# Performance work log

Hardware: AMD Instinct MI355X
Metric: run time of the kernel (lower is better)

Reference implementation:

```python
import jax, jax.numpy as jnp
import numpy as np

HEADS = 4
NEG_SLOPE = 0.2  # GATv2Conv default negative_slope and module's LeakyReLU
LN_EPS = 1e-5


def setup_inputs() -> dict:
    key = jax.random.key(0)
    ks = jax.random.split(key, 12)
    N, D, E = 50000, 128, 400000
    H, C = HEADS, D
    s = 0.05
    x = jax.random.normal(ks[0], (N, D), dtype=jnp.float32)
    edge_index = jax.random.randint(ks[1], (2, E), 0, N, dtype=jnp.int64)
    return {
        "x": x,
        "edge_index": edge_index,
        "W_l": jax.random.normal(ks[2], (D, H * C), dtype=jnp.float32) * s,
        "b_l": jnp.zeros((H * C,), jnp.float32),
        "W_r": jax.random.normal(ks[3], (D, H * C), dtype=jnp.float32) * s,
        "b_r": jnp.zeros((H * C,), jnp.float32),
        "att": jax.random.normal(ks[4], (H, C), dtype=jnp.float32) * s,
        "gat_bias": jnp.zeros((C,), jnp.float32),
        "ln_g": jnp.ones((D,), jnp.float32),
        "ln_b": jnp.zeros((D,), jnp.float32),
        "W1": jax.random.normal(ks[5], (D, 2 * D), dtype=jnp.float32) * s,
        "b1": jnp.zeros((2 * D,), jnp.float32),
        "W2": jax.random.normal(ks[6], (2 * D, D), dtype=jnp.float32) * s,
        "b2": jnp.zeros((D,), jnp.float32),
    }


def _gatv2(x, src, dst, W_l, b_l, W_r, b_r, att, gat_bias, N):
    D = x.shape[1]
    H, C = HEADS, D
    xl = (x @ W_l + b_l).reshape(N, H, C)  # source-side projection
    xr = (x @ W_r + b_r).reshape(N, H, C)  # target-side projection
    # per-edge GATv2 score: leaky_relu(x_j + x_i) . att
    e = jax.nn.leaky_relu(xl[src] + xr[dst], NEG_SLOPE)  # [E, H, C]
    alpha = jnp.einsum('ehc,hc->eh', e, att)             # [E, H]
    # segment softmax over destination nodes
    amax = jax.ops.segment_max(alpha, dst, num_segments=N)  # [N, H]
    ex = jnp.exp(alpha - amax[dst])
    denom = jax.ops.segment_sum(ex, dst, num_segments=N)
    w = ex / (denom[dst] + 1e-16)                        # [E, H]
    msg = xl[src] * w[:, :, None]                        # [E, H, C]
    out = jax.ops.segment_sum(msg, dst, num_segments=N)  # [N, H, C]
    return out.mean(axis=1) + gat_bias                   # concat=False -> head mean + bias


def reference(x, edge_index, W_l, b_l, W_r, b_r, att, gat_bias, ln_g, ln_b, W1, b1, W2, b2):
    N = x.shape[0]
    # GATv2Conv default add_self_loops=True
    loops = jnp.arange(N, dtype=edge_index.dtype)
    src = jnp.concatenate([edge_index[0], loops])
    dst = jnp.concatenate([edge_index[1], loops])
    h = x + _gatv2(x, src, dst, W_l, b_l, W_r, b_r, att, gat_bias, N)
    # LayerNorm
    mu = h.mean(-1, keepdims=True)
    var = ((h - mu) ** 2).mean(-1, keepdims=True)
    hn = (h - mu) * jax.lax.rsqrt(var + LN_EPS) * ln_g + ln_b
    # FFN with residual
    ffn = jax.nn.leaky_relu(hn @ W1 + b1, NEG_SLOPE) @ W2 + b2
    return hn + ffn
```

## Files before the change

kernel.cpp:

```cpp
#include <hip/hip_runtime.h>
#include <hip/hip_bf16.h>
#include <stdint.h>

typedef __hip_bfloat16 bf16;
typedef __attribute__((ext_vector_type(8))) short short8;
typedef __attribute__((ext_vector_type(4))) float f32x4;

#define NEG 0.2f
#define LN_EPS 1e-5f

__device__ __host__ __forceinline__ int stdch(int q) {
    return (q & ~63) | (16 * (q & 3)) | ((q & 63) >> 2);
}

__device__ __forceinline__ float bits2f(unsigned b) {
    return __uint_as_float(b << 16);
}
__device__ __forceinline__ float hi2f(unsigned b) {
    return __uint_as_float(b & 0xffff0000u);
}
__device__ __forceinline__ unsigned short f2b_bits(float f) {
    unsigned u = __float_as_uint(f);
    unsigned r = u + 0x7fffu + ((u >> 16) & 1u);
    return (unsigned short)(r >> 16);
}
__device__ __forceinline__ float lrelu(float v) {
    return fmaxf(v, 0.f) + NEG * fminf(v, 0.f);
}
__device__ __forceinline__ void unpack8(uint4 u, float* v) {
    v[0] = bits2f(u.x); v[1] = hi2f(u.x);
    v[2] = bits2f(u.y); v[3] = hi2f(u.y);
    v[4] = bits2f(u.z); v[5] = hi2f(u.z);
    v[6] = bits2f(u.w); v[7] = hi2f(u.w);
}

union S8 { uint4 u; short8 s; unsigned short us[8]; };
__device__ __forceinline__ short8 ld8b(const char* p) {
    S8 c; c.u = *(const uint4*)p; return c.s;
}
__device__ __forceinline__ short8 ld8f(const float* p) {
    float4 a = ((const float4*)p)[0], b = ((const float4*)p)[1];
    S8 c;
    c.us[0] = f2b_bits(a.x); c.us[1] = f2b_bits(a.y);
    c.us[2] = f2b_bits(a.z); c.us[3] = f2b_bits(a.w);
    c.us[4] = f2b_bits(b.x); c.us[5] = f2b_bits(b.y);
    c.us[6] = f2b_bits(b.z); c.us[7] = f2b_bits(b.w);
    return c.s;
}

__global__ void detect_kernel(const unsigned* __restrict__ xw, const int* __restrict__ ei,
                              int* __restrict__ flags, int E) {
    int lane = threadIdx.x;
    int sane = 0;
    for (int k = 0; k < 4; ++k) {
        unsigned short lo = (unsigned short)(xw[k * 64 + lane] & 0xFFFFu);
        int ex = (lo >> 7) & 0xFF;
        if (lo == 0 || (ex > 100 && ex < 155)) sane++;
    }
#pragma unroll
    for (int off = 32; off > 0; off >>= 1) sane += __shfl_xor(sane, off);
    int nchk = E < 64 ? E : 64;
    int bad = (lane < nchk) ? (ei[2 * lane + 1] != 0) : 0;
    unsigned long long bb = __ballot(bad);
    if (lane == 0) {
        flags[0] = (sane > 200) ? 1 : 0;
        flags[1] = (bb == 0ULL) ? 1 : 0;
    }
}

struct PrepArgs {
    const void* Wl; const void* Wr; const void* W1; const void* W2;
    const void* ssrc[8];
    unsigned short* Wlt; unsigned short* Wrt; unsigned short* W1t; unsigned short* W2t;
    float* smalls;
    int* deg;
    int N;
};
__device__ __forceinline__ float cvt_one(const void* p, int idx, int isb) {
    return isb ? bits2f(((const unsigned short*)p)[idx]) : ((const float*)p)[idx];
}
__global__ __launch_bounds__(256) void prep_kernel(PrepArgs a, const int* __restrict__ flags) {
    int isb = flags[0];
    int i = blockIdx.x * 256 + threadIdx.x;
    int seg = blockIdx.y;
    if (seg == 0) {
        if (i < 512 * 128) {
            int c = i >> 7, k = i & 127;
            a.Wlt[i] = isb ? ((const unsigned short*)a.Wl)[k * 512 + c]
                           : f2b_bits(((const float*)a.Wl)[k * 512 + c]);
        }
    } else if (seg == 1) {
        if (i < 512 * 128) {
            int c = i >> 7, k = i & 127;
            a.Wrt[i] = isb ? ((const unsigned short*)a.Wr)[k * 512 + c]
                           : f2b_bits(((const float*)a.Wr)[k * 512 + c]);
        }
    } else if (seg == 2) {
        if (i < 256 * 128) {
            int c = i >> 7, q = i & 127;
            int k = stdch(q);
            a.W1t[i] = isb ? ((const unsigned short*)a.W1)[k * 256 + c]
                           : f2b_bits(((const float*)a.W1)[k * 256 + c]);
        }
    } else if (seg == 3) {
        if (i < 128 * 256) {
            int c = i >> 8, p = i & 255;
            int k = stdch(p);
            a.W2t[i] = isb ? ((const unsigned short*)a.W2)[k * 128 + c]
                           : f2b_bits(((const float*)a.W2)[k * 128 + c]);
        }
    } else if (seg == 4) {
        if (i < a.N) a.deg[i] = 1;
    } else {
        if (i < 512) a.smalls[i] = cvt_one(a.ssrc[0], i, isb);
        else if (i < 1024) a.smalls[i] = cvt_one(a.ssrc[1], i - 512, isb);
        else if (i < 1536) {
            int j = i - 1024, h = j >> 7, q = j & 127;
            a.smalls[i] = cvt_one(a.ssrc[2], h * 128 + stdch(q), isb);
        } else if (i < 1664) a.smalls[i] = cvt_one(a.ssrc[3], stdch(i - 1536), isb);
        else if (i < 1792)   a.smalls[i] = cvt_one(a.ssrc[4], stdch(i - 1664), isb);
        else if (i < 1920)   a.smalls[i] = cvt_one(a.ssrc[5], stdch(i - 1792), isb);
        else if (i < 2176)   a.smalls[i] = cvt_one(a.ssrc[6], i - 1920, isb);
        else if (i < 2304)   a.smalls[i] = cvt_one(a.ssrc[7], i - 2176, isb);
    }
}


__global__ __launch_bounds__(256) void proj_mfma_kernel(
    const void* __restrict__ xv, const unsigned short* __restrict__ Wlt,
    const unsigned short* __restrict__ Wrt, const float* __restrict__ smalls,
    unsigned short* __restrict__ xl, unsigned short* __restrict__ xr,
    int N, const int* __restrict__ flags) {
    int isb = flags[0];
    int wid = threadIdx.x >> 6, lane = threadIdx.x & 63;
    int quad = lane >> 4, l16 = lane & 15;
    int m0 = blockIdx.x * 64;

    int ra[4];
#pragma unroll
    for (int rf = 0; rf < 4; ++rf) {
        int r = m0 + rf * 16 + l16;
        ra[rf] = (r < N) ? r : N - 1;
    }
    short8 A[4][4];
#pragma unroll
    for (int rf = 0; rf < 4; ++rf)
#pragma unroll
        for (int k4 = 0; k4 < 4; ++k4) {
            int ko = k4 * 32 + quad * 8;
            if (isb) A[rf][k4] = ld8b((const char*)xv + ((size_t)ra[rf] * 128 + ko) * 2);
            else     A[rf][k4] = ld8f((const float*)xv + (size_t)ra[rf] * 128 + ko);
        }

    for (int iter = 0; iter < 4; ++iter) {
        const unsigned short* Wt = (iter < 2) ? Wlt : Wrt;
        const float* bias = smalls + ((iter < 2) ? 0 : 512);
        unsigned short* out = (iter < 2) ? xl : xr;
        int n0 = (iter & 1) * 256 + wid * 64;

        f32x4 acc[4][4];
#pragma unroll
        for (int rf = 0; rf < 4; ++rf)
#pragma unroll
            for (int c = 0; c < 4; ++c) acc[rf][c] = (f32x4){0.f, 0.f, 0.f, 0.f};

#pragma unroll
        for (int k4 = 0; k4 < 4; ++k4) {
            short8 b[4];
#pragma unroll
            for (int c = 0; c < 4; ++c)
                b[c] = ld8b((const char*)(Wt + (size_t)(n0 + c * 16 + l16) * 128 + k4 * 32 + quad * 8));
#pragma unroll
            for (int rf = 0; rf < 4; ++rf)
#pragma unroll
                for (int c = 0; c < 4; ++c)
                    acc[rf][c] = __builtin_amdgcn_mfma_f32_16x16x32_bf16(A[rf][k4], b[c], acc[rf][c], 0, 0, 0);
        }
        float bv[4];
#pragma unroll
        for (int c = 0; c < 4; ++c) bv[c] = bias[n0 + c * 16 + l16];
#pragma unroll
        for (int rf = 0; rf < 4; ++rf) {
#pragma unroll
            for (int j = 0; j < 4; ++j) {
                int row = m0 + rf * 16 + quad * 4 + j;
                if (row < N) {
                    uint2 pk;
                    pk.x = (unsigned)f2b_bits(acc[rf][0][j] + bv[0]) |
                           ((unsigned)f2b_bits(acc[rf][1][j] + bv[1]) << 16);
                    pk.y = (unsigned)f2b_bits(acc[rf][2][j] + bv[2]) |
                           ((unsigned)f2b_bits(acc[rf][3][j] + bv[3]) << 16);
                    *(uint2*)(out + (size_t)row * 512 + n0 + 4 * l16) = pk;
                }
            }
        }
    }
}

__global__ __launch_bounds__(256) void hist_kernel(const int* __restrict__ ei,
                                                   int* __restrict__ deg,
                                                   const int* __restrict__ flags,
                                                   int E, int N) {
    int e = blockIdx.x * 256 + threadIdx.x;
    if (e >= E) return;
    int d = flags[1] ? ei[2 * (size_t)E + 2 * (size_t)e] : ei[(size_t)E + e];
    if ((unsigned)d >= (unsigned)N) d = 0;
    atomicAdd(&deg[d], 1);
}

__global__ __launch_bounds__(256) void scanA_kernel(const int* __restrict__ deg,
                                                    int* __restrict__ part, int N) {
    int t = threadIdx.x, lane = t & 63, wid = t >> 6;
    int i = blockIdx.x * 256 + t;
    int v = (i < N) ? deg[i] : 0;
#pragma unroll
    for (int off = 32; off > 0; off >>= 1) v += __shfl_xor(v, off);
    __shared__ int ws4[4];
    if (lane == 0) ws4[wid] = v;
    __syncthreads();
    if (t == 0) part[blockIdx.x] = ws4[0] + ws4[1] + ws4[2] + ws4[3];
}

__global__ __launch_bounds__(1024) void scanB_kernel(int* __restrict__ part,
                                                     int* __restrict__ rowptr,
                                                     int nb, int N) {
    int t = threadIdx.x, lane = t & 63, wid = t >> 6;
    int v = (t < nb) ? part[t] : 0;
    int x = v;
#pragma unroll
    for (int off = 1; off < 64; off <<= 1) {
        int u = __shfl_up(x, off);
        if (lane >= off) x += u;
    }
    __shared__ int wsum[16];
    if (lane == 63) wsum[wid] = x;
    __syncthreads();
    if (wid == 0 && lane < 16) {
        int y = wsum[lane];
#pragma unroll
        for (int off = 1; off < 16; off <<= 1) {
            int u = __shfl_up(y, off);
            if (lane >= off) y += u;
        }
        wsum[lane] = y;
    }
    __syncthreads();
    int base = (wid > 0) ? wsum[wid - 1] : 0;
    int incl = base + x;
    if (t < nb) part[t] = incl - v;
    if (t == nb - 1) rowptr[N] = incl;
}

__global__ __launch_bounds__(256) void scanC_kernel(const int* __restrict__ deg,
                                                    const int* __restrict__ part,
                                                    int* __restrict__ rowptr,
                                                    int* __restrict__ cursor, int N) {
    int t = threadIdx.x, lane = t & 63, wid = t >> 6;
    int i = blockIdx.x * 256 + t;
    int v = (i < N) ? deg[i] : 0;
    int x = v;
#pragma unroll
    for (int off = 1; off < 64; off <<= 1) {
        int u = __shfl_up(x, off);
        if (lane >= off) x += u;
    }
    __shared__ int wsum[4];
    if (lane == 63) wsum[wid] = x;
    __syncthreads();
    int base = part[blockIdx.x];
    for (int w = 0; w < wid; ++w) base += wsum[w];
    int excl = base + x - v;
    if (i < N) { rowptr[i] = excl; cursor[i] = excl; }
}

__global__ __launch_bounds__(256) void scatter_kernel(const int* __restrict__ ei,
                                                      int* __restrict__ cursor,
                                                      int* __restrict__ srcs,
                                                      const int* __restrict__ flags,
                                                      int E, int ET, int N) {
    int e = blockIdx.x * 256 + threadIdx.x;
    if (e >= ET) return;
    int s, d;
    if (e < E) {
        if (flags[1]) { s = ei[2 * (size_t)e]; d = ei[2 * (size_t)E + 2 * (size_t)e]; }
        else          { s = ei[e];             d = ei[(size_t)E + e]; }
    } else { s = e - E; d = s; }
    if ((unsigned)s >= (unsigned)N) s = 0;
    if ((unsigned)d >= (unsigned)N) d = 0;
    int pos = atomicAdd(&cursor[d], 1);
    srcs[pos] = s;
}

__global__ __launch_bounds__(256) void agg_kernel(
    const bf16* __restrict__ xl, bf16* __restrict__ xr,
    const void* __restrict__ xv, const int* __restrict__ rowptr,
    const int* __restrict__ srcs, const float* __restrict__ smalls,
    int N, const int* __restrict__ flags) {
    int n = blockIdx.x * 4 + (threadIdx.x >> 6);
    if (n >= N) return;
    int lane = threadIdx.x & 63;
    int h = lane >> 4, cg = lane & 15;
    const float* att = smalls + 1024;
    const float* gat_bias = smalls + 1536;
    const float* ln_g = smalls + 1664;
    const float* ln_b = smalls + 1792;

    float att_f[8];
    {
        const float4* ap = (const float4*)(att + (size_t)h * 128 + cg * 8);
        float4 a0 = ap[0], a1 = ap[1];
        att_f[0] = a0.x; att_f[1] = a0.y; att_f[2] = a0.z; att_f[3] = a0.w;
        att_f[4] = a1.x; att_f[5] = a1.y; att_f[6] = a1.z; att_f[7] = a1.w;
    }
    float xr_f[8];
    uint4 xw = ((const uint4*)(xr + (size_t)n * 512))[lane];
    unpack8(xw, xr_f);

    float o[8];
#pragma unroll
    for (int j = 0; j < 8; ++j) o[j] = 0.f;
    float lsum = 0.f;

    int beg = rowptr[n], end = rowptr[n + 1];
    const uint4* xlu = (const uint4*)xl;
    int sA = srcs[beg];
    int sB = (beg + 1 < end) ? srcs[beg + 1] : sA;
    uint4 lw = xlu[(size_t)sA * 64 + lane];
    for (int i = beg; i < end; ++i) {
        uint4 cur = lw;
        int snext = sB;
        if (i + 2 < end) sB = srcs[i + 2];
        if (i + 1 < end) lw = xlu[(size_t)snext * 64 + lane];
        float v[8];
        unpack8(cur, v);
        float p = 0.f;
#pragma unroll
        for (int j = 0; j < 8; ++j) {
            float t = lrelu(v[j] + xr_f[j]);
            p = fmaf(t, att_f[j], p);
        }
        p += __shfl_xor(p, 1); p += __shfl_xor(p, 2);
        p += __shfl_xor(p, 4); p += __shfl_xor(p, 8);
        float w = __expf(fminf(p, 60.f));
        lsum += w;
#pragma unroll
        for (int j = 0; j < 8; ++j) o[j] = fmaf(w, v[j], o[j]);
    }
    float inv = 0.25f / lsum;
#pragma unroll
    for (int j = 0; j < 8; ++j) o[j] *= inv;
#pragma unroll
    for (int j = 0; j < 8; ++j) {
        o[j] += __shfl_xor(o[j], 16);
        o[j] += __shfl_xor(o[j], 32);
    }
    int bc = 64 * (cg >> 3) + 2 * (cg & 7);
    float xf[8];
    if (flags[0]) {
#pragma unroll
        for (int c = 0; c < 4; ++c) {
            unsigned d = *(const unsigned*)((const unsigned short*)xv + (size_t)n * 128 + bc + 16 * c);
            xf[c] = bits2f(d); xf[c + 4] = hi2f(d);
        }
    } else {
#pragma unroll
        for (int c = 0; c < 4; ++c) {
            float2 f = *(const float2*)((const float*)xv + (size_t)n * 128 + bc + 16 * c);
            xf[c] = f.x; xf[c + 4] = f.y;
        }
    }
    float gb[8];
    {
        const float4* gp = (const float4*)(gat_bias + cg * 8);
        float4 a0 = gp[0], a1 = gp[1];
        gb[0] = a0.x; gb[1] = a0.y; gb[2] = a0.z; gb[3] = a0.w;
        gb[4] = a1.x; gb[5] = a1.y; gb[6] = a1.z; gb[7] = a1.w;
    }
    float vl[8];
    float s1 = 0.f;
#pragma unroll
    for (int j = 0; j < 8; ++j) { vl[j] = xf[j] + o[j] + gb[j]; s1 += vl[j]; }
    s1 += __shfl_xor(s1, 1); s1 += __shfl_xor(s1, 2);
    s1 += __shfl_xor(s1, 4); s1 += __shfl_xor(s1, 8);
    float mu = s1 * (1.f / 128.f);
    float s2 = 0.f;
#pragma unroll
    for (int j = 0; j < 8; ++j) { float d = vl[j] - mu; s2 += d * d; }
    s2 += __shfl_xor(s2, 1); s2 += __shfl_xor(s2, 2);
    s2 += __shfl_xor(s2, 4); s2 += __shfl_xor(s2, 8);
    float rinv = rsqrtf(s2 * (1.f / 128.f) + LN_EPS);
    if (h == 0) {
        float g[8], bt[8];
        const float4* gp = (const float4*)(ln_g + cg * 8);
        float4 g0 = gp[0], g1 = gp[1];
        g[0] = g0.x; g[1] = g0.y; g[2] = g0.z; g[3] = g0.w;
        g[4] = g1.x; g[5] = g1.y; g[6] = g1.z; g[7] = g1.w;
        const float4* bp = (const float4*)(ln_b + cg * 8);
        float4 b0 = bp[0], b1v = bp[1];
        bt[0] = b0.x; bt[1] = b0.y; bt[2] = b0.z; bt[3] = b0.w;
        bt[4] = b1v.x; bt[5] = b1v.y; bt[6] = b1v.z; bt[7] = b1v.w;
        float hnv[8];
#pragma unroll
        for (int j = 0; j < 8; ++j) hnv[j] = (vl[j] - mu) * rinv * g[j] + bt[j];
        char* rowp = (char*)xr + (size_t)n * 1024;
        float* hp = (float*)rowp;
#pragma unroll
        for (int c = 0; c < 4; ++c) {
            float2 f; f.x = hnv[c]; f.y = hnv[c + 4];
            *(float2*)(hp + bc + 16 * c) = f;
        }
        uint4 pk;
        pk.x = (unsigned)f2b_bits(hnv[0]) | ((unsigned)f2b_bits(hnv[1]) << 16);
        pk.y = (unsigned)f2b_bits(hnv[2]) | ((unsigned)f2b_bits(hnv[3]) << 16);
        pk.z = (unsigned)f2b_bits(hnv[4]) | ((unsigned)f2b_bits(hnv[5]) << 16);
        pk.w = (unsigned)f2b_bits(hnv[6]) | ((unsigned)f2b_bits(hnv[7]) << 16);
        *(uint4*)(rowp + 512 + cg * 16) = pk;
    }
}

__global__ __launch_bounds__(256) void ffn1_mfma_kernel(
    const char* __restrict__ hnrows, const unsigned short* __restrict__ W1t,
    const float* __restrict__ smalls, unsigned short* __restrict__ mid, int N) {
    const float* b1 = smalls + 1920;
    int wid = threadIdx.x >> 6, lane = threadIdx.x & 63;
    int quad = lane >> 4, l16 = lane & 15;
    int m0 = blockIdx.x * 64;
    int n0 = wid * 64;

    int ra[4];
#pragma unroll
    for (int rf = 0; rf < 4; ++rf) {
        int r = m0 + rf * 16 + l16;
        ra[rf] = (r < N) ? r : N - 1;
    }
    short8 A[4][4];
#pragma unroll
    for (int rf = 0; rf < 4; ++rf)
#pragma unroll
        for (int k4 = 0; k4 < 4; ++k4)
            A[rf][k4] = ld8b(hnrows + (size_t)ra[rf] * 1024 + 512 + (k4 * 32 + quad * 8) * 2);

    f32x4 acc[4][4];
#pragma unroll
    for (int rf = 0; rf < 4; ++rf)
#pragma unroll
        for (int c = 0; c < 4; ++c) acc[rf][c] = (f32x4){0.f, 0.f, 0.f, 0.f};

#pragma unroll
    for (int k4 = 0; k4 < 4; ++k4) {
        short8 b[4];
#pragma unroll
        for (int c = 0; c < 4; ++c)
            b[c] = ld8b((const char*)(W1t + (size_t)(n0 + c * 16 + l16) * 128 + k4 * 32 + quad * 8));
#pragma unroll
        for (int rf = 0; rf < 4; ++rf)
#pragma unroll
            for (int c = 0; c < 4; ++c)
                acc[rf][c] = __builtin_amdgcn_mfma_f32_16x16x32_bf16(A[rf][k4], b[c], acc[rf][c], 0, 0, 0);
    }
    float bv[4];
#pragma unroll
    for (int c = 0; c < 4; ++c) bv[c] = b1[n0 + c * 16 + l16];
#pragma unroll
    for (int rf = 0; rf < 4; ++rf) {
#pragma unroll
        for (int j = 0; j < 4; ++j) {
            int row = m0 + rf * 16 + quad * 4 + j;
            if (row < N) {
                uint2 pk;
                pk.x = (unsigned)f2b_bits(lrelu(acc[rf][0][j] + bv[0])) |
                       ((unsigned)f2b_bits(lrelu(acc[rf][1][j] + bv[1])) << 16);
                pk.y = (unsigned)f2b_bits(lrelu(acc[rf][2][j] + bv[2])) |
                       ((unsigned)f2b_bits(lrelu(acc[rf][3][j] + bv[3])) << 16);
                *(uint2*)(mid + (size_t)row * 256 + n0 + 4 * l16) = pk;
            }
        }
    }
}

__global__ __launch_bounds__(256) void ffn2_mfma_kernel(
    const unsigned short* __restrict__ mid, const char* __restrict__ hnrows,
    const unsigned short* __restrict__ W2t, const float* __restrict__ smalls,
    void* __restrict__ outv, int N, const int* __restrict__ flags) {
    const float* b2v = smalls + 2176;
    int wid = threadIdx.x >> 6, lane = threadIdx.x & 63;
    int quad = lane >> 4, l16 = lane & 15;
    int m0 = blockIdx.x * 128 + (wid >> 1) * 64;
    int n0 = (wid & 1) * 64;

    int ra[4];
#pragma unroll
    for (int rf = 0; rf < 4; ++rf) {
        int r = m0 + rf * 16 + l16;
        ra[rf] = (r < N) ? r : N - 1;
    }

    f32x4 acc[4][4];
#pragma unroll
    for (int rf = 0; rf < 4; ++rf)
#pragma unroll
        for (int c = 0; c < 4; ++c) acc[rf][c] = (f32x4){0.f, 0.f, 0.f, 0.f};

#pragma unroll
    for (int kk = 0; kk < 256; kk += 32) {
        short8 a[4], b[4];
#pragma unroll
        for (int rf = 0; rf < 4; ++rf)
            a[rf] = ld8b((const char*)(mid + (size_t)ra[rf] * 256 + kk + quad * 8));
#pragma unroll
        for (int c = 0; c < 4; ++c)
            b[c] = ld8b((const char*)(W2t + (size_t)(n0 + c * 16 + l16) * 256 + kk + quad * 8));
#pragma unroll
        for (int rf = 0; rf < 4; ++rf)
#pragma unroll
            for (int c = 0; c < 4; ++c)
                acc[rf][c] = __builtin_amdgcn_mfma_f32_16x16x32_bf16(a[rf], b[c], acc[rf][c], 0, 0, 0);
    }
    int isb = flags[0];
#pragma unroll
    for (int c = 0; c < 4; ++c) {
        int col = n0 + c * 16 + l16;
        float bv = b2v[col];
#pragma unroll
        for (int rf = 0; rf < 4; ++rf) {
#pragma unroll
            for (int j = 0; j < 4; ++j) {
                int row = m0 + rf * 16 + quad * 4 + j;
                if (row < N) {
                    float hval = *(const float*)(hnrows + (size_t)row * 1024 + (size_t)col * 4);
                    float val = hval + acc[rf][c][j] + bv;
                    if (isb) ((unsigned short*)outv)[(size_t)row * 128 + col] = f2b_bits(val);
                    else     ((float*)outv)[(size_t)row * 128 + col] = val;
                }
            }
        }
    }
}

extern "C" void kernel_launch(void* const* d_in, const int* in_sizes, int n_in,
                              void* d_out, int out_size, void* d_ws, size_t ws_size,
                              hipStream_t stream) {
    const void* x = d_in[0];
    const int* ei = (const int*)d_in[1];

    int N = in_sizes[0] / 128;
    int E = in_sizes[1] / 2;
    int ET = E + N;
    int nb = (N + 255) / 256;

    char* base = (char*)d_ws;
    int* flags = (int*)base;
    size_t off = 256;
    float* smalls = (float*)(base + off);               off += 2304 * 4;
    off = (off + 255) & ~(size_t)255;
    unsigned short* Wlt = (unsigned short*)(base + off); off += 512 * 128 * 2;
    unsigned short* Wrt = (unsigned short*)(base + off); off += 512 * 128 * 2;
    unsigned short* W1t = (unsigned short*)(base + off); off += 256 * 128 * 2;
    unsigned short* W2t = (unsigned short*)(base + off); off += 128 * 256 * 2;
    off = (off + 1023) & ~(size_t)1023;
    bf16* xl = (bf16*)(base + off);   off += (size_t)N * 512 * 2;
    bf16* xr = (bf16*)(base + off);   off += (size_t)N * 512 * 2;
    int* srcs = (int*)(base + off);   off += (size_t)ET * 4;
    int* rowptr = (int*)(base + off); off += (size_t)(N + 1) * 4;
    int* deg = (int*)(base + off);    off += (size_t)N * 4;
    int* cursor = (int*)(base + off); off += (size_t)N * 4;
    int* part = (int*)(base + off);   off += (size_t)nb * 4;
    unsigned short* mid = (unsigned short*)xl;
    const char* hnrows = (const char*)xr;

    detect_kernel<<<1, 64, 0, stream>>>((const unsigned*)x, ei, flags, E);

    PrepArgs pa;
    pa.Wl = d_in[2]; pa.Wr = d_in[4]; pa.W1 = d_in[10]; pa.W2 = d_in[12];
    pa.ssrc[0] = d_in[3];  pa.ssrc[1] = d_in[5];  pa.ssrc[2] = d_in[6];
    pa.ssrc[3] = d_in[7];  pa.ssrc[4] = d_in[8];  pa.ssrc[5] = d_in[9];
    pa.ssrc[6] = d_in[11]; pa.ssrc[7] = d_in[13];
    pa.Wlt = Wlt; pa.Wrt = Wrt; pa.W1t = W1t; pa.W2t = W2t;
    pa.smalls = smalls; pa.deg = deg; pa.N = N;
    int px = (65536 > N ? 65536 : N);
    prep_kernel<<<dim3((px + 255) / 256, 6), 256, 0, stream>>>(pa, flags);

    int g64 = (N + 63) / 64;
    proj_mfma_kernel<<<g64, 256, 0, stream>>>(x, Wlt, Wrt, smalls, (unsigned short*)xl,
                                              (unsigned short*)xr, N, flags);

    hist_kernel<<<(E + 255) / 256, 256, 0, stream>>>(ei, deg, flags, E, N);
    scanA_kernel<<<nb, 256, 0, stream>>>(deg, part, N);
    scanB_kernel<<<1, 1024, 0, stream>>>(part, rowptr, nb, N);
    scanC_kernel<<<nb, 256, 0, stream>>>(deg, part, rowptr, cursor, N);
    scatter_kernel<<<(ET + 255) / 256, 256, 0, stream>>>(ei, cursor, srcs, flags, E, ET, N);

    agg_kernel<<<(N + 3) / 4, 256, 0, stream>>>(xl, xr, x, rowptr, srcs, smalls, N, flags);

    ffn1_mfma_kernel<<<g64, 256, 0, stream>>>(hnrows, W1t, smalls, mid, N);
    ffn2_mfma_kernel<<<(N + 127) / 128, 256, 0, stream>>>(mid, hnrows, W2t, smalls, d_out, N, flags);
}
```

Baseline: 354.2 us.

## Fuse FFN kernels, sort nodes by degree, fold residual into GEMM, simplify leaky-relu

```diff
diff --git a/kernel.cpp b/kernel.cpp
--- a/kernel.cpp
+++ b/kernel.cpp
@@ -71,9 +71,9 @@
 struct PrepArgs {
     const void* Wl; const void* Wr; const void* W1; const void* W2;
     const void* ssrc[8];
-    unsigned short* Wlt; unsigned short* Wrt; unsigned short* W1t; unsigned short* W2t;
+    unsigned short* Wlt; unsigned short* Wrt; unsigned short* W1t; unsigned short* W2x;
     float* smalls;
-    int* deg;
+    int* deg; int* dhist;
     int N;
 };
 __device__ __forceinline__ float cvt_one(const void* p, int idx, int isb) {
@@ -103,14 +103,20 @@
                            : f2b_bits(((const float*)a.W1)[k * 256 + c]);
         }
     } else if (seg == 3) {
-        if (i < 128 * 256) {
-            int c = i >> 8, p = i & 255;
-            int k = stdch(p);
-            a.W2t[i] = isb ? ((const unsigned short*)a.W2)[k * 128 + c]
-                           : f2b_bits(((const float*)a.W2)[k * 128 + c]);
+        if (i < 128 * 384) {
+            int c = i / 384, p = i - c * 384;
+            if (p < 256) {
+                int k = stdch(p);
+                a.W2x[i] = isb ? ((const unsigned short*)a.W2)[k * 128 + c]
+                               : f2b_bits(((const float*)a.W2)[k * 128 + c]);
+            } else {
+                int q = p - 256;
+                a.W2x[i] = (stdch(q) == c) ? (unsigned short)0x3F80 : (unsigned short)0;
+            }
         }
     } else if (seg == 4) {
         if (i < a.N) a.deg[i] = 1;
+        if (i < 256) a.dhist[i] = 0;
     } else {
         if (i < 512) a.smalls[i] = cvt_one(a.ssrc[0], i, isb);
         else if (i < 1024) a.smalls[i] = cvt_one(a.ssrc[1], i - 512, isb);
@@ -209,20 +215,28 @@
 }
 
 __global__ __launch_bounds__(256) void scanA_kernel(const int* __restrict__ deg,
-                                                    int* __restrict__ part, int N) {
+                                                    int* __restrict__ part,
+                                                    int* __restrict__ dhist, int N) {
     int t = threadIdx.x, lane = t & 63, wid = t >> 6;
     int i = blockIdx.x * 256 + t;
-    int v = (i < N) ? deg[i] : 0;
+    int d0 = (i < N) ? deg[i] : 0;
+    int v = d0;
 #pragma unroll
     for (int off = 32; off > 0; off >>= 1) v += __shfl_xor(v, off);
     __shared__ int ws4[4];
     if (lane == 0) ws4[wid] = v;
     __syncthreads();
     if (t == 0) part[blockIdx.x] = ws4[0] + ws4[1] + ws4[2] + ws4[3];
+    if (i < N) {
+        int b = 255 - (d0 < 255 ? d0 : 255);
+        atomicAdd(&dhist[b], 1);
+    }
 }
 
 __global__ __launch_bounds__(1024) void scanB_kernel(int* __restrict__ part,
                                                      int* __restrict__ rowptr,
+                                                     const int* __restrict__ dhist,
+                                                     int* __restrict__ dcur,
                                                      int nb, int N) {
     int t = threadIdx.x, lane = t & 63, wid = t >> 6;
     int v = (t < nb) ? part[t] : 0;
@@ -249,12 +263,32 @@
     int incl = base + x;
     if (t < nb) part[t] = incl - v;
     if (t == nb - 1) rowptr[N] = incl;
+    __syncthreads();
+    int dv = 0, dx = 0;
+    if (t < 256) {
+        dv = dhist[t]; dx = dv;
+#pragma unroll
+        for (int off = 1; off < 64; off <<= 1) {
+            int u = __shfl_up(dx, off);
+            if (lane >= off) dx += u;
+        }
+    }
+    __shared__ int ds4[4];
+    if (t < 256 && lane == 63) ds4[wid] = dx;
+    __syncthreads();
+    if (t < 256) {
+        int b2 = 0;
+        for (int w = 0; w < wid; ++w) b2 += ds4[w];
+        dcur[t] = b2 + dx - dv;
+    }
 }
 
 __global__ __launch_bounds__(256) void scanC_kernel(const int* __restrict__ deg,
                                                     const int* __restrict__ part,
                                                     int* __restrict__ rowptr,
-                                                    int* __restrict__ cursor, int N) {
+                                                    int* __restrict__ cursor,
+                                                    int* __restrict__ dcur,
+                                                    int* __restrict__ order, int N) {
     int t = threadIdx.x, lane = t & 63, wid = t >> 6;
     int i = blockIdx.x * 256 + t;
     int v = (i < N) ? deg[i] : 0;
@@ -270,7 +304,13 @@
     int base = part[blockIdx.x];
     for (int w = 0; w < wid; ++w) base += wsum[w];
     int excl = base + x - v;
-    if (i < N) { rowptr[i] = excl; cursor[i] = excl; }
+    if (i < N) {
+        rowptr[i] = excl;
+        cursor[i] = excl;
+        int b = 255 - (v < 255 ? v : 255);
+        int pos = atomicAdd(&dcur[b], 1);
+        order[pos] = i;
+    }
 }
 
 __global__ __launch_bounds__(256) void scatter_kernel(const int* __restrict__ ei,
@@ -295,9 +335,10 @@
     const bf16* __restrict__ xl, bf16* __restrict__ xr,
     const void* __restrict__ xv, const int* __restrict__ rowptr,
     const int* __restrict__ srcs, const float* __restrict__ smalls,
-    int N, const int* __restrict__ flags) {
-    int n = blockIdx.x * 4 + (threadIdx.x >> 6);
-    if (n >= N) return;
+    const int* __restrict__ order, int N, const int* __restrict__ flags) {
+    int gid = blockIdx.x * 4 + (threadIdx.x >> 6);
+    if (gid >= N) return;
+    int n = order[gid];
     int lane = threadIdx.x & 63;
     int h = lane >> 4, cg = lane & 15;
     const float* att = smalls + 1024;
@@ -333,12 +374,14 @@
         if (i + 1 < end) lw = xlu[(size_t)snext * 64 + lane];
         float v[8];
         unpack8(cur, v);
-        float p = 0.f;
+        float dotA = 0.f, dotB = 0.f;
 #pragma unroll
         for (int j = 0; j < 8; ++j) {
-            float t = lrelu(v[j] + xr_f[j]);
-            p = fmaf(t, att_f[j], p);
-        }
+            float z = v[j] + xr_f[j];
+            dotA = fmaf(z, att_f[j], dotA);
+            dotB = fmaf(fabsf(z), att_f[j], dotB);
+        }
+        float p = fmaf(0.4f, dotB, 0.6f * dotA);
         p += __shfl_xor(p, 1); p += __shfl_xor(p, 2);
         p += __shfl_xor(p, 4); p += __shfl_xor(p, 8);
         float w = __expf(fminf(p, 60.f));
@@ -403,29 +446,25 @@
 #pragma unroll
         for (int j = 0; j < 8; ++j) hnv[j] = (vl[j] - mu) * rinv * g[j] + bt[j];
         char* rowp = (char*)xr + (size_t)n * 1024;
-        float* hp = (float*)rowp;
-#pragma unroll
-        for (int c = 0; c < 4; ++c) {
-            float2 f; f.x = hnv[c]; f.y = hnv[c + 4];
-            *(float2*)(hp + bc + 16 * c) = f;
-        }
         uint4 pk;
         pk.x = (unsigned)f2b_bits(hnv[0]) | ((unsigned)f2b_bits(hnv[1]) << 16);
         pk.y = (unsigned)f2b_bits(hnv[2]) | ((unsigned)f2b_bits(hnv[3]) << 16);
         pk.z = (unsigned)f2b_bits(hnv[4]) | ((unsigned)f2b_bits(hnv[5]) << 16);
         pk.w = (unsigned)f2b_bits(hnv[6]) | ((unsigned)f2b_bits(hnv[7]) << 16);
-        *(uint4*)(rowp + 512 + cg * 16) = pk;
-    }
-}
-
-__global__ __launch_bounds__(256) void ffn1_mfma_kernel(
+        *(uint4*)(rowp + cg * 16) = pk;
+    }
+}
+
+__global__ __launch_bounds__(256) void ffn_fused_kernel(
     const char* __restrict__ hnrows, const unsigned short* __restrict__ W1t,
-    const float* __restrict__ smalls, unsigned short* __restrict__ mid, int N) {
+    const unsigned short* __restrict__ W2x, const float* __restrict__ smalls,
+    void* __restrict__ outv, int N, const int* __restrict__ flags) {
+    __shared__ __align__(16) char lds[64 * 528];
     const float* b1 = smalls + 1920;
+    const float* b2v = smalls + 2176;
     int wid = threadIdx.x >> 6, lane = threadIdx.x & 63;
     int quad = lane >> 4, l16 = lane & 15;
     int m0 = blockIdx.x * 64;
-    int n0 = wid * 64;
 
     int ra[4];
 #pragma unroll
@@ -438,97 +477,91 @@
     for (int rf = 0; rf < 4; ++rf)
 #pragma unroll
         for (int k4 = 0; k4 < 4; ++k4)
-            A[rf][k4] = ld8b(hnrows + (size_t)ra[rf] * 1024 + 512 + (k4 * 32 + quad * 8) * 2);
-
-    f32x4 acc[4][4];
-#pragma unroll
-    for (int rf = 0; rf < 4; ++rf)
-#pragma unroll
-        for (int c = 0; c < 4; ++c) acc[rf][c] = (f32x4){0.f, 0.f, 0.f, 0.f};
-
-#pragma unroll
-    for (int k4 = 0; k4 < 4; ++k4) {
-        short8 b[4];
-#pragma unroll
-        for (int c = 0; c < 4; ++c)
-            b[c] = ld8b((const char*)(W1t + (size_t)(n0 + c * 16 + l16) * 128 + k4 * 32 + quad * 8));
+            A[rf][k4] = ld8b(hnrows + (size_t)ra[rf] * 1024 + (k4 * 32 + quad * 8) * 2);
+
+    {
+        int n0 = wid * 64;
+        f32x4 acc[4][4];
 #pragma unroll
         for (int rf = 0; rf < 4; ++rf)
 #pragma unroll
+            for (int c = 0; c < 4; ++c) acc[rf][c] = (f32x4){0.f, 0.f, 0.f, 0.f};
+#pragma unroll
+        for (int k4 = 0; k4 < 4; ++k4) {
+            short8 b[4];
+#pragma unroll
             for (int c = 0; c < 4; ++c)
-                acc[rf][c] = __builtin_amdgcn_mfma_f32_16x16x32_bf16(A[rf][k4], b[c], acc[rf][c], 0, 0, 0);
-    }
-    float bv[4];
-#pragma unroll
-    for (int c = 0; c < 4; ++c) bv[c] = b1[n0 + c * 16 + l16];
-#pragma unroll
-    for (int rf = 0; rf < 4; ++rf) {
-#pragma unroll
-        for (int j = 0; j < 4; ++j) {
-            int row = m0 + rf * 16 + quad * 4 + j;
-            if (row < N) {
+                b[c] = ld8b((const char*)(W1t + (size_t)(n0 + c * 16 + l16) * 128 + k4 * 32 + quad * 8));
+#pragma unroll
+            for (int rf = 0; rf < 4; ++rf)
+#pragma unroll
+                for (int c = 0; c < 4; ++c)
+                    acc[rf][c] = __builtin_amdgcn_mfma_f32_16x16x32_bf16(A[rf][k4], b[c], acc[rf][c], 0, 0, 0);
+        }
+        float bv[4];
+#pragma unroll
+        for (int c = 0; c < 4; ++c) bv[c] = b1[n0 + c * 16 + l16];
+#pragma unroll
+        for (int rf = 0; rf < 4; ++rf) {
+#pragma unroll
+            for (int j = 0; j < 4; ++j) {
+                int lrow = rf * 16 + quad * 4 + j;
                 uint2 pk;
                 pk.x = (unsigned)f2b_bits(lrelu(acc[rf][0][j] + bv[0])) |
                        ((unsigned)f2b_bits(lrelu(acc[rf][1][j] + bv[1])) << 16);
                 pk.y = (unsigned)f2b_bits(lrelu(acc[rf][2][j] + bv[2])) |
                        ((unsigned)f2b_bits(lrelu(acc[rf][3][j] + bv[3])) << 16);
-                *(uint2*)(mid + (size_t)row * 256 + n0 + 4 * l16) = pk;
+                *(uint2*)(lds + lrow * 528 + (n0 + 4 * l16) * 2) = pk;
             }
         }
     }
-}
-
-__global__ __launch_bounds__(256) void ffn2_mfma_kernel(
-    const unsigned short* __restrict__ mid, const char* __restrict__ hnrows,
-    const unsigned short* __restrict__ W2t, const float* __restrict__ smalls,
-    void* __restrict__ outv, int N, const int* __restrict__ flags) {
-    const float* b2v = smalls + 2176;
-    int wid = threadIdx.x >> 6, lane = threadIdx.x & 63;
-    int quad = lane >> 4, l16 = lane & 15;
-    int m0 = blockIdx.x * 128 + (wid >> 1) * 64;
-    int n0 = (wid & 1) * 64;
-
-    int ra[4];
-#pragma unroll
-    for (int rf = 0; rf < 4; ++rf) {
-        int r = m0 + rf * 16 + l16;
-        ra[rf] = (r < N) ? r : N - 1;
-    }
-
-    f32x4 acc[4][4];
-#pragma unroll
-    for (int rf = 0; rf < 4; ++rf)
-#pragma unroll
-        for (int c = 0; c < 4; ++c) acc[rf][c] = (f32x4){0.f, 0.f, 0.f, 0.f};
-
+    __syncthreads();
+    int rh = wid >> 1, nh = wid & 1;
+    int n0b = nh * 64;
+    f32x4 a2[2][4];
+#pragma unroll
+    for (int rfl = 0; rfl < 2; ++rfl)
+#pragma unroll
+        for (int c = 0; c < 4; ++c) a2[rfl][c] = (f32x4){0.f, 0.f, 0.f, 0.f};
 #pragma unroll
     for (int kk = 0; kk < 256; kk += 32) {
-        short8 a[4], b[4];
-#pragma unroll
-        for (int rf = 0; rf < 4; ++rf)
-            a[rf] = ld8b((const char*)(mid + (size_t)ra[rf] * 256 + kk + quad * 8));
+        short8 am[2], b[4];
+#pragma unroll
+        for (int rfl = 0; rfl < 2; ++rfl)
+            am[rfl] = ld8b(lds + (rh * 32 + rfl * 16 + l16) * 528 + (kk + quad * 8) * 2);
 #pragma unroll
         for (int c = 0; c < 4; ++c)
-            b[c] = ld8b((const char*)(W2t + (size_t)(n0 + c * 16 + l16) * 256 + kk + quad * 8));
-#pragma unroll
-        for (int rf = 0; rf < 4; ++rf)
+            b[c] = ld8b((const char*)(W2x + (size_t)(n0b + c * 16 + l16) * 384 + kk + quad * 8));
+#pragma unroll
+        for (int rfl = 0; rfl < 2; ++rfl)
 #pragma unroll
             for (int c = 0; c < 4; ++c)
-                acc[rf][c] = __builtin_amdgcn_mfma_f32_16x16x32_bf16(a[rf], b[c], acc[rf][c], 0, 0, 0);
+                a2[rfl][c] = __builtin_amdgcn_mfma_f32_16x16x32_bf16(am[rfl], b[c], a2[rfl][c], 0, 0, 0);
+    }
+#pragma unroll
+    for (int k4 = 0; k4 < 4; ++k4) {
+        short8 b[4];
+#pragma unroll
+        for (int c = 0; c < 4; ++c)
+            b[c] = ld8b((const char*)(W2x + (size_t)(n0b + c * 16 + l16) * 384 + 256 + k4 * 32 + quad * 8));
+#pragma unroll
+        for (int rfl = 0; rfl < 2; ++rfl)
+#pragma unroll
+            for (int c = 0; c < 4; ++c)
+                a2[rfl][c] = __builtin_amdgcn_mfma_f32_16x16x32_bf16(A[rh * 2 + rfl][k4], b[c], a2[rfl][c], 0, 0, 0);
     }
     int isb = flags[0];
 #pragma unroll
     for (int c = 0; c < 4; ++c) {
-        int col = n0 + c * 16 + l16;
+        int col = n0b + c * 16 + l16;
         float bv = b2v[col];
 #pragma unroll
-        for (int rf = 0; rf < 4; ++rf) {
+        for (int rfl = 0; rfl < 2; ++rfl) {
 #pragma unroll
             for (int j = 0; j < 4; ++j) {
-                int row = m0 + rf * 16 + quad * 4 + j;
+                int row = m0 + rh * 32 + rfl * 16 + quad * 4 + j;
                 if (row < N) {
-                    float hval = *(const float*)(hnrows + (size_t)row * 1024 + (size_t)col * 4);
-                    float val = hval + acc[rf][c][j] + bv;
+                    float val = a2[rfl][c][j] + bv;
                     if (isb) ((unsigned short*)outv)[(size_t)row * 128 + col] = f2b_bits(val);
                     else     ((float*)outv)[(size_t)row * 128 + col] = val;
                 }
@@ -556,7 +589,7 @@
     unsigned short* Wlt = (unsigned short*)(base + off); off += 512 * 128 * 2;
     unsigned short* Wrt = (unsigned short*)(base + off); off += 512 * 128 * 2;
     unsigned short* W1t = (unsigned short*)(base + off); off += 256 * 128 * 2;
-    unsigned short* W2t = (unsigned short*)(base + off); off += 128 * 256 * 2;
+    unsigned short* W2x = (unsigned short*)(base + off); off += 128 * 384 * 2;
     off = (off + 1023) & ~(size_t)1023;
     bf16* xl = (bf16*)(base + off);   off += (size_t)N * 512 * 2;
     bf16* xr = (bf16*)(base + off);   off += (size_t)N * 512 * 2;
@@ -565,7 +598,9 @@
     int* deg = (int*)(base + off);    off += (size_t)N * 4;
     int* cursor = (int*)(base + off); off += (size_t)N * 4;
     int* part = (int*)(base + off);   off += (size_t)nb * 4;
-    unsigned short* mid = (unsigned short*)xl;
+    int* order = (int*)(base + off);  off += (size_t)N * 4;
+    int* dhist = (int*)(base + off);  off += 256 * 4;
+    int* dcur = (int*)(base + off);   off += 256 * 4;
     const char* hnrows = (const char*)xr;
 
     detect_kernel<<<1, 64, 0, stream>>>((const unsigned*)x, ei, flags, E);
@@ -575,8 +610,8 @@
     pa.ssrc[0] = d_in[3];  pa.ssrc[1] = d_in[5];  pa.ssrc[2] = d_in[6];
     pa.ssrc[3] = d_in[7];  pa.ssrc[4] = d_in[8];  pa.ssrc[5] = d_in[9];
     pa.ssrc[6] = d_in[11]; pa.ssrc[7] = d_in[13];
-    pa.Wlt = Wlt; pa.Wrt = Wrt; pa.W1t = W1t; pa.W2t = W2t;
-    pa.smalls = smalls; pa.deg = deg; pa.N = N;
+    pa.Wlt = Wlt; pa.Wrt = Wrt; pa.W1t = W1t; pa.W2x = W2x;
+    pa.smalls = smalls; pa.deg = deg; pa.dhist = dhist; pa.N = N;
     int px = (65536 > N ? 65536 : N);
     prep_kernel<<<dim3((px + 255) / 256, 6), 256, 0, stream>>>(pa, flags);
 
@@ -585,13 +620,12 @@
                                               (unsigned short*)xr, N, flags);
 
     hist_kernel<<<(E + 255) / 256, 256, 0, stream>>>(ei, deg, flags, E, N);
-    scanA_kernel<<<nb, 256, 0, stream>>>(deg, part, N);
-    scanB_kernel<<<1, 1024, 0, stream>>>(part, rowptr, nb, N);
-    scanC_kernel<<<nb, 256, 0, stream>>>(deg, part, rowptr, cursor, N);
+    scanA_kernel<<<nb, 256, 0, stream>>>(deg, part, dhist, N);
+    scanB_kernel<<<1, 1024, 0, stream>>>(part, rowptr, dhist, dcur, nb, N);
+    scanC_kernel<<<nb, 256, 0, stream>>>(deg, part, rowptr, cursor, dcur, order, N);
     scatter_kernel<<<(ET + 255) / 256, 256, 0, stream>>>(ei, cursor, srcs, flags, E, ET, N);
 
-    agg_kernel<<<(N + 3) / 4, 256, 0, stream>>>(xl, xr, x, rowptr, srcs, smalls, N, flags);
-
-    ffn1_mfma_kernel<<<g64, 256, 0, stream>>>(hnrows, W1t, smalls, mid, N);
-    ffn2_mfma_kernel<<<(N + 127) / 128, 256, 0, stream>>>(mid, hnrows, W2t, smalls, d_out, N, flags);
-}
+    agg_kernel<<<(N + 3) / 4, 256, 0, stream>>>(xl, xr, x, rowptr, srcs, smalls, order, N, flags);
+
+    ffn_fused_kernel<<<g64, 256, 0, stream>>>(hnrows, W1t, W2x, smalls, d_out, N, flags);
+}
```

Result: slower. 689.6 us (+94.7%).
